# Performance work log

Measured on AMD Instinct MI355X. Metric: run time of the kernel, lower is better.

Reference implementation:

```python
import jax, jax.numpy as jnp
import numpy as np

H = 768
NH = 12
HD = 64
FF = 3072
EPS = 1e-12


def layer_norm(x, g, b):
    mu = jnp.mean(x, axis=-1, keepdims=True)
    var = jnp.mean((x - mu) ** 2, axis=-1, keepdims=True)
    return (x - mu) * jax.lax.rsqrt(var + EPS) * g + b


def setup_inputs() -> dict:
    key = jax.random.key(0)
    ks = jax.random.split(key, 16)
    B, S, L = 16, 512, 50
    s = 0.02
    return {
        "hidden_states": jax.random.normal(ks[0], (B, S, H), jnp.float32),
        "attention_mask": jnp.zeros((B, 1, 1, S), jnp.float32),
        "past_key": jax.random.normal(ks[1], (B, NH, L, HD), jnp.float32),
        "past_value": jax.random.normal(ks[2], (B, NH, L, HD), jnp.float32),
        "Wq": jax.random.normal(ks[3], (H, H), jnp.float32) * s,
        "bq": jnp.zeros((H,), jnp.float32),
        "Wk": jax.random.normal(ks[4], (H, H), jnp.float32) * s,
        "bk": jnp.zeros((H,), jnp.float32),
        "Wv": jax.random.normal(ks[5], (H, H), jnp.float32) * s,
        "bv": jnp.zeros((H,), jnp.float32),
        "Wo": jax.random.normal(ks[6], (H, H), jnp.float32) * s,
        "bo": jnp.zeros((H,), jnp.float32),
        "ln1_g": jnp.ones((H,), jnp.float32),
        "ln1_b": jnp.zeros((H,), jnp.float32),
        "Wi": jax.random.normal(ks[7], (H, FF), jnp.float32) * s,
        "bi": jnp.zeros((FF,), jnp.float32),
        "Wf": jax.random.normal(ks[8], (FF, H), jnp.float32) * s,
        "bf": jnp.zeros((H,), jnp.float32),
        "ln2_g": jnp.ones((H,), jnp.float32),
        "ln2_b": jnp.zeros((H,), jnp.float32),
    }


def reference(hidden_states, attention_mask, past_key, past_value,
              Wq, bq, Wk, bk, Wv, bv, Wo, bo, ln1_g, ln1_b,
              Wi, bi, Wf, bf, ln2_g, ln2_b):
    B, S, _ = hidden_states.shape
    L = past_key.shape[2]

    def heads(x):  # [B,S,H] -> [B,NH,S,HD]
        return x.reshape(B, S, NH, HD).transpose(0, 2, 1, 3)

    q = heads(hidden_states @ Wq + bq)
    k = heads(hidden_states @ Wk + bk)
    v = heads(hidden_states @ Wv + bv)

    # faithful to source bug: past_key_values[0] concatenated into BOTH k and v
    k = jnp.concatenate([past_key, k], axis=2)  # [B,NH,L+S,HD]
    v = jnp.concatenate([past_key, v], axis=2)

    scores = jnp.einsum('bhqd,bhkd->bhqk', q, k) / jnp.sqrt(jnp.float32(HD))
    # visual mask positions get +1.0 (torch.ones), faithful to source
    vis_mask = jnp.ones((B, 1, 1, L), scores.dtype)
    full_mask = jnp.concatenate([vis_mask, attention_mask], axis=-1)
    scores = scores + full_mask

    probs = jax.nn.softmax(scores, axis=-1)
    ctx = jnp.einsum('bhqk,bhkd->bhqd', probs, v)  # [B,NH,S,HD]
    ctx = ctx.transpose(0, 2, 1, 3).reshape(B, S, H)

    attn_out = layer_norm(ctx @ Wo + bo + hidden_states, ln1_g, ln1_b)

    inter = jax.nn.gelu(attn_out @ Wi + bi, approximate=False)
    layer_out = layer_norm(inter @ Wf + bf + attn_out, ln2_g, ln2_b)
    return layer_out
```

## Files before the change

kernel.cpp:

```cpp
#include <hip/hip_runtime.h>
#include <math.h>

#define HDIM 64
#define NHEAD 12
#define HDN 768
#define QKVN 2304
#define FFDIM 3072
#define LPAST 50
#define SEQ 512
#define NBATCH 16
#define TKV (LPAST + SEQ)
#define TKVP 576
#define MTOK (NBATCH * SEQ)
#define NBH (NBATCH * NHEAD)

typedef __attribute__((ext_vector_type(8))) short short8;
typedef __attribute__((ext_vector_type(4))) float f32x4;

__device__ __forceinline__ ushort f2bf(float x) {
    union { float f; unsigned u; } c; c.f = x;
    unsigned r = (c.u + 0x7fffu + ((c.u >> 16) & 1u)) >> 16;
    return (ushort)r;
}
__device__ __forceinline__ float bf2f(ushort u) { return __uint_as_float((unsigned)u << 16); }
__device__ __forceinline__ float geluf(float v) {
    return 0.5f * v * (1.0f + erff(v * 0.70710678118654752f));
}

#define GLOAD_LDS16(gsrc, ldst)                                                    \
    __builtin_amdgcn_global_load_lds(                                              \
        (const __attribute__((address_space(1))) void*)(gsrc),                     \
        (__attribute__((address_space(3))) void*)(ldst), 16, 0, 0)

__global__ __launch_bounds__(256) void prep(
    const float* __restrict__ hs, ushort* __restrict__ hs_bf,
    const float* __restrict__ bq, const float* __restrict__ bk,
    const float* __restrict__ bv, float* __restrict__ bqkv,
    const float* __restrict__ Wq, const float* __restrict__ Wk,
    const float* __restrict__ Wv, const float* __restrict__ Wo,
    ushort* __restrict__ WqT, ushort* __restrict__ WkT,
    ushort* __restrict__ WvT, ushort* __restrict__ WoT,
    const float* __restrict__ Wi, ushort* __restrict__ WiT,
    const float* __restrict__ Wf, ushort* __restrict__ WfT)
{
    __shared__ float tls[32][33];
    int bid = blockIdx.x;
    const int tid = threadIdx.x;

    if (bid < 6144) {
        int i = bid * 256 + tid;
        float4 v = ((const float4*)hs)[i];
        ushort4 o; o.x = f2bf(v.x); o.y = f2bf(v.y); o.z = f2bf(v.z); o.w = f2bf(v.w);
        ((ushort4*)hs_bf)[i] = o;
        return;
    }
    bid -= 6144;
    if (bid < 9) {
        int i = bid * 256 + tid;
        bqkv[i] = i < HDN ? bq[i] : (i < 2 * HDN ? bk[i - HDN] : bv[i - 2 * HDN]);
        return;
    }
    bid -= 9;

    const float* W; ushort* WT; int K, N, bx, by;
    if (bid < 2304) {
        int z = bid / 576, r = bid % 576;
        W = z == 0 ? Wq : z == 1 ? Wk : z == 2 ? Wv : Wo;
        WT = z == 0 ? WqT : z == 1 ? WkT : z == 2 ? WvT : WoT;
        K = HDN; N = HDN; bx = r % 24; by = r / 24;
    } else if (bid < 4608) {
        int r = bid - 2304; W = Wi; WT = WiT; K = HDN; N = FFDIM; bx = r % 96; by = r / 96;
    } else {
        int r = bid - 4608; W = Wf; WT = WfT; K = FFDIM; N = HDN; bx = r % 24; by = r / 24;
    }
    const int n0 = bx * 32, k0 = by * 32;
    const int tx = tid & 31, ty = tid >> 5;
    #pragma unroll
    for (int i = 0; i < 4; ++i)
        tls[ty + i * 8][tx] = W[(size_t)(k0 + ty + i * 8) * N + n0 + tx];
    __syncthreads();
    #pragma unroll
    for (int i = 0; i < 4; ++i)
        WT[(size_t)(n0 + ty + i * 8) * K + k0 + tx] = f2bf(tls[tx][ty + i * 8]);
}

template<int EPI, int BN>
__global__ __launch_bounds__(256, BN == 64 ? 4 : 2) void gemm_t(
    const ushort* __restrict__ A, const ushort* __restrict__ B,
    int lda, int ldb,
    const float* __restrict__ bias, const float* __restrict__ resid,
    const ushort* __restrict__ resid_bf,
    ushort* __restrict__ Cout, int M, int N, int K)
{
    constexpr int NF = BN / 32;
    constexpr int NBG = BN / 64;
    constexpr int BUFU = 4096 + BN * 32;
    __shared__ ushort sm[3 * BUFU];

    const int tid = threadIdx.x;
    const int lane = tid & 63;
    const int wv = tid >> 6;
    const int wr = wv >> 1, wc = wv & 1;
    const int bm = blockIdx.x * 128, bn = blockIdx.y * BN;
    const int lr = lane & 15, lg = lane >> 4;
    const int swzu = ((lr * 64 + lg * 16) ^ ((lr & 8) << 2)) >> 1;

    int arow[2], akk[2], brow[NBG], bkk[NBG];
    #pragma unroll
    for (int r = 0; r < 2; ++r) {
        int o = (tid + 256 * r) * 16;
        int st = o >> 10, q = o & 1023;
        q ^= ((q >> 9) & 1) << 5;
        arow[r] = st * 16 + (q >> 6);
        akk[r] = (q & 63) >> 1;
    }
    #pragma unroll
    for (int r = 0; r < NBG; ++r) {
        int o = (tid + 256 * r) * 16;
        int st = o >> 10, q = o & 1023;
        q ^= ((q >> 9) & 1) << 5;
        brow[r] = st * 16 + (q >> 6);
        bkk[r] = (q & 63) >> 1;
    }
    const ushort* Abase = A + (size_t)bm * lda;
    const ushort* Bbase = B + (size_t)bn * ldb;
    const int nt = K >> 5;

    f32x4 acc[4][NF] = {};

#define STAGE(T, BUF)                                                            \
    do {                                                                         \
        const int k0_ = (T) << 5;                                                \
        char* base_ = (char*)(sm + (BUF) * BUFU);                                \
        _Pragma("unroll")                                                        \
        for (int r_ = 0; r_ < 2; ++r_)                                           \
            GLOAD_LDS16(Abase + (size_t)arow[r_] * lda + k0_ + akk[r_],          \
                        base_ + (tid + 256 * r_) * 16);                          \
        _Pragma("unroll")                                                        \
        for (int r_ = 0; r_ < NBG; ++r_)                                         \
            GLOAD_LDS16(Bbase + (size_t)brow[r_] * ldb + k0_ + bkk[r_],          \
                        base_ + 8192 + (tid + 256 * r_) * 16);                   \
    } while (0)

    STAGE(0, 0);
    STAGE(1, 1);
    if (BN == 128) asm volatile("s_waitcnt vmcnt(4)" ::: "memory");
    else           asm volatile("s_waitcnt vmcnt(3)" ::: "memory");
    __builtin_amdgcn_sched_barrier(0);
    __builtin_amdgcn_s_barrier();
    __builtin_amdgcn_sched_barrier(0);

    int buf = 0;
    for (int t = 0; t < nt; ++t) {
        if (t + 2 < nt) {
            int nbuf = buf + 2; if (nbuf >= 3) nbuf -= 3;
            STAGE(t + 2, nbuf);
        }
        const ushort* ab = sm + buf * BUFU;
        short8 af[4], bfv[NF];
        #pragma unroll
        for (int i = 0; i < 4; ++i)
            af[i] = *(const short8*)(ab + (wr * 4 + i) * 512 + swzu);
        #pragma unroll
        for (int j = 0; j < NF; ++j)
            bfv[j] = *(const short8*)(ab + 4096 + (wc * NF + j) * 512 + swzu);
        __builtin_amdgcn_s_setprio(1);
        #pragma unroll
        for (int i = 0; i < 4; ++i)
            #pragma unroll
            for (int j = 0; j < NF; ++j)
                acc[i][j] = __builtin_amdgcn_mfma_f32_16x16x32_bf16(
                    af[i], bfv[j], acc[i][j], 0, 0, 0);
        __builtin_amdgcn_s_setprio(0);
        if (t + 2 < nt) {
            if (BN == 128) asm volatile("s_waitcnt vmcnt(4)" ::: "memory");
            else           asm volatile("s_waitcnt vmcnt(3)" ::: "memory");
        } else {
            asm volatile("s_waitcnt vmcnt(0)" ::: "memory");
        }
        __builtin_amdgcn_sched_barrier(0);
        __builtin_amdgcn_s_barrier();
        __builtin_amdgcn_sched_barrier(0);
        buf = buf + 1 == 3 ? 0 : buf + 1;
    }
#undef STAGE

    #pragma unroll
    for (int i = 0; i < 4; ++i) {
        #pragma unroll
        for (int j = 0; j < NF; ++j) {
            const int col = bn + wc * (BN / 2) + j * 16 + lr;
            const float bv = bias[col];
            #pragma unroll
            for (int rr = 0; rr < 4; ++rr) {
                const int row = bm + wr * 64 + i * 16 + lg * 4 + rr;
                const size_t idx = (size_t)row * N + col;
                float v = acc[i][j][rr] + bv;
                if (EPI == 1) v += resid[idx];
                if (EPI == 4) v += bf2f(resid_bf[idx]);
                if (EPI == 2) v = geluf(v);
                Cout[idx] = f2bf(v);
            }
        }
    }
}

__global__ __launch_bounds__(256) void kvAll(
    const ushort* __restrict__ qkv, const float* __restrict__ past_key,
    ushort* __restrict__ kf, ushort* __restrict__ vt)
{
    __shared__ ushort td[64][72];
    const int bh = blockIdx.x / 9;
    const int t0 = (blockIdx.x % 9) * 64;
    const int b = bh / NHEAD, h = bh % NHEAD;
    const int trow = threadIdx.x >> 2, seg = threadIdx.x & 3;
    const int t = t0 + trow;

    ushort kv16[16], vv16[16];
    if (t < LPAST) {
        const float* pk = past_key + ((size_t)bh * LPAST + t) * HDIM + seg * 16;
        #pragma unroll
        for (int i = 0; i < 4; ++i) {
            float4 f = ((const float4*)pk)[i];
            kv16[i * 4 + 0] = f2bf(f.x); kv16[i * 4 + 1] = f2bf(f.y);
            kv16[i * 4 + 2] = f2bf(f.z); kv16[i * 4 + 3] = f2bf(f.w);
        }
        #pragma unroll
        for (int i = 0; i < 16; ++i) vv16[i] = kv16[i];
    } else if (t < TKV) {
        const ushort* kp = qkv + ((size_t)(b * SEQ + (t - LPAST))) * QKVN
                               + HDN + h * HDIM + seg * 16;
        *(uint4*)&kv16[0] = ((const uint4*)kp)[0];
        *(uint4*)&kv16[8] = ((const uint4*)kp)[1];
        const ushort* vp = kp + HDN;
        *(uint4*)&vv16[0] = ((const uint4*)vp)[0];
        *(uint4*)&vv16[8] = ((const uint4*)vp)[1];
    } else {
        #pragma unroll
        for (int i = 0; i < 16; ++i) { kv16[i] = 0; vv16[i] = 0; }
    }

    if (t < TKV) {
        ushort* kd = kf + (((size_t)bh * TKV + t) << 6) + seg * 16;
        *(uint4*)kd = *(uint4*)&kv16[0];
        *(uint4*)(kd + 8) = *(uint4*)&kv16[8];
    }

    #pragma unroll
    for (int i = 0; i < 16; ++i) td[trow][seg * 16 + i] = vv16[i];
    __syncthreads();

    const int d = threadIdx.x >> 2;
    ushort o[16];
    #pragma unroll
    for (int i = 0; i < 16; ++i) o[i] = td[seg * 16 + i][d];
    ushort* dst = vt + ((size_t)bh * HDIM + d) * TKVP + t0 + seg * 16;
    *(uint4*)dst = *(uint4*)&o[0];
    *(uint4*)(dst + 8) = *(uint4*)&o[8];
}

__global__ __launch_bounds__(256) void attn4(
    const ushort* __restrict__ qkv, const ushort* __restrict__ kf,
    const ushort* __restrict__ vt, const float* __restrict__ mask,
    ushort* __restrict__ ctx)
{
    __shared__ ushort Ks[64 * 64];
    __shared__ ushort Vs[64 * 64];
    __shared__ ushort Ps[4][16 * 64];

    const int wv = threadIdx.x >> 6, lane = threadIdx.x & 63;
    const int lr = lane & 15, lg = lane >> 4;
    const int bid = blockIdx.x;
    const int xcd = bid & 7, gi = bid >> 3;
    const int bh = xcd * (NBH / 8) + (gi >> 3);
    const int s0 = (gi & 7) * 64;
    const int b = bh / NHEAD, h = bh % NHEAD;

    short8 af[2];
    {
        const ushort* qp = qkv + ((size_t)(b * SEQ + s0 + wv * 16 + lr)) * QKVN
                               + h * HDIM + lg * 8;
        af[0] = *(const short8*)qp;
        af[1] = *(const short8*)(qp + 32);
    }

    const ushort* kbase = kf + (size_t)bh * TKV * HDIM;
    const ushort* vbase = vt + (size_t)bh * HDIM * TKVP;

    float l[4] = {};
    f32x4 ctxa[4] = {};

    for (int kt = 0; kt < 9; ++kt) {
        const int t0 = kt * 64;
        #pragma unroll
        for (int r = 0; r < 2; ++r) {
            int sl = (int)threadIdx.x + 256 * r;
            int row = sl >> 3, p = sl & 7;
            int j = p ^ (row & 7);
            int trow = t0 + row; if (trow > TKV - 1) trow = TKV - 1;
            GLOAD_LDS16(kbase + ((size_t)trow << 6) + j * 8, (char*)Ks + sl * 16);
        }
        #pragma unroll
        for (int r = 0; r < 2; ++r) {
            int sl = (int)threadIdx.x + 256 * r;
            int row = sl >> 3, p = sl & 7;
            int j = p ^ (row & 7);
            GLOAD_LDS16(vbase + (size_t)row * TKVP + t0 + j * 8, (char*)Vs + sl * 16);
        }
        __syncthreads();

        f32x4 sa[4] = {};
        #pragma unroll
        for (int kb = 0; kb < 4; ++kb) {
            const int key = kb * 16 + lr;
            #pragma unroll
            for (int c = 0; c < 2; ++c) {
                const int phys = (c * 4 + lg) ^ (key & 7);
                short8 kfrag = *(const short8*)&Ks[key * 64 + phys * 8];
                sa[kb] = __builtin_amdgcn_mfma_f32_16x16x32_bf16(
                    af[c], kfrag, sa[kb], 0, 0, 0);
            }
        }

        #pragma unroll
        for (int kb = 0; kb < 4; ++kb) {
            const int t = t0 + kb * 16 + lr;
            float addv;
            if (t >= TKV) addv = -1e30f;
            else addv = ((t < LPAST) ? 1.0f : mask[(size_t)b * SEQ + (t - LPAST)]) - 4.0f;
            const int key = kb * 16 + lr;
            #pragma unroll
            for (int r = 0; r < 4; ++r) {
                float p = __expf(fmaf(sa[kb][r], 0.125f, addv));
                l[r] += p;
                const int q_ = lg * 4 + r;
                const int phys = (key >> 3) ^ (q_ & 7);
                Ps[wv][q_ * 64 + phys * 8 + (key & 7)] = f2bf(p);
            }
        }

        short8 pa[2];
        #pragma unroll
        for (int c = 0; c < 2; ++c) {
            const int phys = (c * 4 + lg) ^ (lr & 7);
            pa[c] = *(const short8*)&Ps[wv][lr * 64 + phys * 8];
        }
        #pragma unroll
        for (int dg = 0; dg < 4; ++dg) {
            const int d = dg * 16 + lr;
            #pragma unroll
            for (int c = 0; c < 2; ++c) {
                const int phys = (c * 4 + lg) ^ (d & 7);
                short8 vfrag = *(const short8*)&Vs[d * 64 + phys * 8];
                ctxa[dg] = __builtin_amdgcn_mfma_f32_16x16x32_bf16(
                    pa[c], vfrag, ctxa[dg], 0, 0, 0);
            }
        }
        __syncthreads();
    }

    #pragma unroll
    for (int r = 0; r < 4; ++r) {
        float s = l[r];
        s += __shfl_xor(s, 1); s += __shfl_xor(s, 2);
        s += __shfl_xor(s, 4); s += __shfl_xor(s, 8);
        l[r] = 1.0f / s;
    }
    #pragma unroll
    for (int r = 0; r < 4; ++r) {
        const int q_ = s0 + wv * 16 + lg * 4 + r;
        const size_t base = ((size_t)(b * SEQ + q_)) * HDN + h * HDIM;
        #pragma unroll
        for (int dg = 0; dg < 4; ++dg)
            ctx[base + dg * 16 + lr] = f2bf(ctxa[dg][r] * l[r]);
    }
}

__global__ __launch_bounds__(256) void layernorm3(
    const ushort* __restrict__ x, const float* __restrict__ g,
    const float* __restrict__ b, float* __restrict__ out,
    ushort* __restrict__ out_bf)
{
    const size_t row = blockIdx.x;
    const ushort* xr = &x[row * HDN];
    const int t = threadIdx.x;

    float v0 = bf2f(xr[t]), v1 = bf2f(xr[t + 256]), v2 = bf2f(xr[t + 512]);

    __shared__ float red[4];
    float s = v0 + v1 + v2;
    #pragma unroll
    for (int off = 32; off > 0; off >>= 1) s += __shfl_xor(s, off);
    if ((t & 63) == 0) red[t >> 6] = s;
    __syncthreads();
    float mean = (red[0] + red[1] + red[2] + red[3]) * (1.0f / 768.0f);

    float d0 = v0 - mean, d1 = v1 - mean, d2 = v2 - mean;
    float vs = d0 * d0 + d1 * d1 + d2 * d2;
    #pragma unroll
    for (int off = 32; off > 0; off >>= 1) vs += __shfl_xor(vs, off);
    __syncthreads();
    if ((t & 63) == 0) red[t >> 6] = vs;
    __syncthreads();
    float var = (red[0] + red[1] + red[2] + red[3]) * (1.0f / 768.0f);
    float rstd = rsqrtf(var + 1e-12f);

    float o0 = d0 * rstd * g[t] + b[t];
    float o1 = d1 * rstd * g[t + 256] + b[t + 256];
    float o2 = d2 * rstd * g[t + 512] + b[t + 512];
    if (out) {
        out[row * HDN + t] = o0;
        out[row * HDN + t + 256] = o1;
        out[row * HDN + t + 512] = o2;
    }
    if (out_bf) {
        out_bf[row * HDN + t] = f2bf(o0);
        out_bf[row * HDN + t + 256] = f2bf(o1);
        out_bf[row * HDN + t + 512] = f2bf(o2);
    }
}

extern "C" void kernel_launch(void* const* d_in, const int* in_sizes, int n_in,
                              void* d_out, int out_size, void* d_ws, size_t ws_size,
                              hipStream_t stream) {
    const float* hs       = (const float*)d_in[0];
    const float* mask     = (const float*)d_in[1];
    const float* past_key = (const float*)d_in[2];
    const float* Wq = (const float*)d_in[4];
    const float* bq = (const float*)d_in[5];
    const float* Wk = (const float*)d_in[6];
    const float* bk = (const float*)d_in[7];
    const float* Wv = (const float*)d_in[8];
    const float* bv = (const float*)d_in[9];
    const float* Wo = (const float*)d_in[10];
    const float* bo = (const float*)d_in[11];
    const float* ln1_g = (const float*)d_in[12];
    const float* ln1_b = (const float*)d_in[13];
    const float* Wi = (const float*)d_in[14];
    const float* bi = (const float*)d_in[15];
    const float* Wf = (const float*)d_in[16];
    const float* bf_ = (const float*)d_in[17];
    const float* ln2_g = (const float*)d_in[18];
    const float* ln2_b = (const float*)d_in[19];
    float* out = (float*)d_out;

    char* w = (char*)d_ws;
    ushort* WqT   = (ushort*)(w + 0);
    ushort* WoT   = (ushort*)(w + 3538944);
    ushort* WiT   = (ushort*)(w + 4718592);
    ushort* WfT   = (ushort*)(w + 9437184);
    float*  bqkv  = (float*)(w + 14155776);
    ushort* hs_bf = (ushort*)(w + 14172160);
    ushort* qkv   = (ushort*)(w + 26755072);
    ushort* kf    = (ushort*)(w + 64503808);
    ushort* vt    = (ushort*)(w + 78315520);
    ushort* ctx_bf = hs_bf;
    ushort* tmp_bf = (ushort*)(w + 64503808);
    ushort* inter  = (ushort*)(w + 14172160);
    ushort* aln_bf = (ushort*)(w + 89669632);
    ushort* WkT = WqT + (size_t)HDN * HDN;
    ushort* WvT = WqT + (size_t)2 * HDN * HDN;

    dim3 b256(256);

    prep<<<dim3(13065), b256, 0, stream>>>(
        hs, hs_bf, bq, bk, bv, bqkv,
        Wq, Wk, Wv, Wo, WqT, WkT, WvT, WoT, Wi, WiT, Wf, WfT);

    gemm_t<0, 128><<<dim3(MTOK / 128, QKVN / 128), b256, 0, stream>>>(
        hs_bf, WqT, HDN, HDN, bqkv, nullptr, nullptr, qkv, MTOK, QKVN, HDN);

    kvAll<<<dim3(NBH * 9), b256, 0, stream>>>(qkv, past_key, kf, vt);

    attn4<<<dim3(NBH * 8), b256, 0, stream>>>(qkv, kf, vt, mask, ctx_bf);

    gemm_t<1, 64><<<dim3(MTOK / 128, HDN / 64), b256, 0, stream>>>(
        ctx_bf, WoT, HDN, HDN, bo, hs, nullptr, tmp_bf, MTOK, HDN, HDN);
    layernorm3<<<dim3(MTOK), b256, 0, stream>>>(tmp_bf, ln1_g, ln1_b, nullptr, aln_bf);

    gemm_t<2, 128><<<dim3(MTOK / 128, FFDIM / 128), b256, 0, stream>>>(
        aln_bf, WiT, HDN, HDN, bi, nullptr, nullptr, inter, MTOK, FFDIM, HDN);
    gemm_t<4, 64><<<dim3(MTOK / 128, HDN / 64), b256, 0, stream>>>(
        inter, WfT, FFDIM, FFDIM, bf_, nullptr, aln_bf, tmp_bf, MTOK, HDN, FFDIM);

    layernorm3<<<dim3(MTOK), b256, 0, stream>>>(tmp_bf, ln2_g, ln2_b, out, nullptr);
}
```

Baseline: 261.3 us.

## Split-K the FFN down-projection GEMM and fuse the partial reduction into LayerNorm

```diff
diff --git a/kernel.cpp b/kernel.cpp
--- a/kernel.cpp
+++ b/kernel.cpp
@@ -104,6 +104,7 @@
     const int bm = blockIdx.x * 128, bn = blockIdx.y * BN;
     const int lr = lane & 15, lg = lane >> 4;
     const int swzu = ((lr * 64 + lg * 16) ^ ((lr & 8) << 2)) >> 1;
+    const size_t kzoff = (size_t)blockIdx.z * K;
 
     int arow[2], akk[2], brow[NBG], bkk[NBG];
     #pragma unroll
@@ -122,8 +123,8 @@
         brow[r] = st * 16 + (q >> 6);
         bkk[r] = (q & 63) >> 1;
     }
-    const ushort* Abase = A + (size_t)bm * lda;
-    const ushort* Bbase = B + (size_t)bn * ldb;
+    const ushort* Abase = A + (size_t)bm * lda + kzoff;
+    const ushort* Bbase = B + (size_t)bn * ldb + kzoff;
     const int nt = K >> 5;
 
     f32x4 acc[4][NF] = {};
@@ -185,12 +186,14 @@
     }
 #undef STAGE
 
+    ushort* Cz = Cout + (size_t)blockIdx.z * M * N;
     #pragma unroll
     for (int i = 0; i < 4; ++i) {
         #pragma unroll
         for (int j = 0; j < NF; ++j) {
             const int col = bn + wc * (BN / 2) + j * 16 + lr;
-            const float bv = bias[col];
+            float bv = 0.0f;
+            if (EPI != 5) bv = bias[col];
             #pragma unroll
             for (int rr = 0; rr < 4; ++rr) {
                 const int row = bm + wr * 64 + i * 16 + lg * 4 + rr;
@@ -199,7 +202,7 @@
                 if (EPI == 1) v += resid[idx];
                 if (EPI == 4) v += bf2f(resid_bf[idx]);
                 if (EPI == 2) v = geluf(v);
-                Cout[idx] = f2bf(v);
+                Cz[idx] = f2bf(v);
             }
         }
     }
@@ -418,6 +421,43 @@
         out_bf[row * HDN + t + 256] = f2bf(o1);
         out_bf[row * HDN + t + 512] = f2bf(o2);
     }
+}
+
+__global__ __launch_bounds__(256) void ln_red(
+    const ushort* __restrict__ p0, const ushort* __restrict__ p1,
+    const float* __restrict__ bias, const ushort* __restrict__ resid,
+    const float* __restrict__ g, const float* __restrict__ b,
+    float* __restrict__ out)
+{
+    const size_t row = blockIdx.x;
+    const size_t base = row * HDN;
+    const int t = threadIdx.x;
+
+    float v0 = bf2f(p0[base + t])       + bf2f(p1[base + t])       + bias[t]       + bf2f(resid[base + t]);
+    float v1 = bf2f(p0[base + t + 256]) + bf2f(p1[base + t + 256]) + bias[t + 256] + bf2f(resid[base + t + 256]);
+    float v2 = bf2f(p0[base + t + 512]) + bf2f(p1[base + t + 512]) + bias[t + 512] + bf2f(resid[base + t + 512]);
+
+    __shared__ float red[4];
+    float s = v0 + v1 + v2;
+    #pragma unroll
+    for (int off = 32; off > 0; off >>= 1) s += __shfl_xor(s, off);
+    if ((t & 63) == 0) red[t >> 6] = s;
+    __syncthreads();
+    float mean = (red[0] + red[1] + red[2] + red[3]) * (1.0f / 768.0f);
+
+    float d0 = v0 - mean, d1 = v1 - mean, d2 = v2 - mean;
+    float vs = d0 * d0 + d1 * d1 + d2 * d2;
+    #pragma unroll
+    for (int off = 32; off > 0; off >>= 1) vs += __shfl_xor(vs, off);
+    __syncthreads();
+    if ((t & 63) == 0) red[t >> 6] = vs;
+    __syncthreads();
+    float var = (red[0] + red[1] + red[2] + red[3]) * (1.0f / 768.0f);
+    float rstd = rsqrtf(var + 1e-12f);
+
+    out[base + t]       = d0 * rstd * g[t]       + b[t];
+    out[base + t + 256] = d1 * rstd * g[t + 256] + b[t + 256];
+    out[base + t + 512] = d2 * rstd * g[t + 512] + b[t + 512];
 }
 
 extern "C" void kernel_launch(void* const* d_in, const int* in_sizes, int n_in,
@@ -457,6 +497,7 @@
     ushort* ctx_bf = hs_bf;
     ushort* tmp_bf = (ushort*)(w + 64503808);
     ushort* inter  = (ushort*)(w + 14172160);
+    ushort* pbuf   = (ushort*)(w + 64503808);
     ushort* aln_bf = (ushort*)(w + 89669632);
     ushort* WkT = WqT + (size_t)HDN * HDN;
     ushort* WvT = WqT + (size_t)2 * HDN * HDN;
@@ -480,8 +521,9 @@
 
     gemm_t<2, 128><<<dim3(MTOK / 128, FFDIM / 128), b256, 0, stream>>>(
         aln_bf, WiT, HDN, HDN, bi, nullptr, nullptr, inter, MTOK, FFDIM, HDN);
-    gemm_t<4, 64><<<dim3(MTOK / 128, HDN / 64), b256, 0, stream>>>(
-        inter, WfT, FFDIM, FFDIM, bf_, nullptr, aln_bf, tmp_bf, MTOK, HDN, FFDIM);
-
-    layernorm3<<<dim3(MTOK), b256, 0, stream>>>(tmp_bf, ln2_g, ln2_b, out, nullptr);
-}
+    gemm_t<5, 128><<<dim3(MTOK / 128, HDN / 128, 2), b256, 0, stream>>>(
+        inter, WfT, FFDIM, FFDIM, nullptr, nullptr, nullptr, pbuf, MTOK, HDN, FFDIM / 2);
+
+    ln_red<<<dim3(MTOK), b256, 0, stream>>>(
+        pbuf, pbuf + (size_t)MTOK * HDN, bf_, aln_bf, ln2_g, ln2_b, out);
+}
```

Result: faster. 245.9 us (-5.9%).
